# Kernel optimization log

Hardware: AMD Instinct MI355X
Metric: run time of the kernel (lower is better)

## Reference

```python
import jax, jax.numpy as jnp
import numpy as np

N = 50000          # nodes
E = 1_600_000      # edges
H = 64             # agg_hidden (heads=1, concat)
IN = 7             # in_channels
EDIM = 4           # edge_dim
G = 256            # num graphs in batch
FC = 128           # fc_hidden
NC = 2             # num_classes
SLOPE = 0.2        # GATv2 LeakyReLU negative slope


def setup_inputs() -> dict:
    key = jax.random.key(0)
    ks = jax.random.split(key, 24)
    s = 0.1
    d = {
        "x": jax.random.normal(ks[0], (N, IN), dtype=jnp.float32),
        "edge_index": jax.random.randint(ks[1], (2, E), 0, N, dtype=jnp.int32),
        "edge_attr": jax.random.normal(ks[2], (E, EDIM), dtype=jnp.float32),
        "batch": jnp.sort(jax.random.randint(ks[3], (N,), 0, G, dtype=jnp.int32)),
        # GATv2 layer 0 (in=7 -> 64)
        "Wl0": jax.random.normal(ks[4], (IN, H)) * s,
        "bl0": jnp.zeros((H,), jnp.float32),
        "Wr0": jax.random.normal(ks[5], (IN, H)) * s,
        "br0": jnp.zeros((H,), jnp.float32),
        "We0": jax.random.normal(ks[6], (EDIM, H)) * s,
        "att0": jax.random.normal(ks[7], (H,)) * s,
        "bias0": jnp.zeros((H,), jnp.float32),
        # GATv2 layer 1 (64 -> 64)
        "Wl1": jax.random.normal(ks[8], (H, H)) * s,
        "bl1": jnp.zeros((H,), jnp.float32),
        "Wr1": jax.random.normal(ks[9], (H, H)) * s,
        "br1": jnp.zeros((H,), jnp.float32),
        "We1": jax.random.normal(ks[10], (EDIM, H)) * s,
        "att1": jax.random.normal(ks[11], (H,)) * s,
        "bias1": jnp.zeros((H,), jnp.float32),
        # MLP head
        "fc1_w": jax.random.normal(ks[12], (H, FC)) * s,
        "fc1_b": jnp.zeros((FC,), jnp.float32),
        "fc2_w": jax.random.normal(ks[13], (FC, NC)) * s,
        "fc2_b": jnp.zeros((NC,), jnp.float32),
    }
    return d


def _gatv2(x, src, dst, edge_attr, Wl, bl, Wr, br, We, att, bias):
    # GATv2Conv (heads=1, concat=True, edge_dim=EDIM), eval mode (no dropout)
    xl = x @ Wl + bl                         # source-side projection [N,H]
    xr = x @ Wr + br                         # target-side projection [N,H]
    e = xl[src] + xr[dst] + edge_attr @ We   # per-edge pre-activation [E,H]
    score = jax.nn.leaky_relu(e, SLOPE) @ att  # [E]
    # segment softmax over destination nodes
    m = jax.ops.segment_max(score, dst, num_segments=N)
    ex = jnp.exp(score - m[dst])
    den = jax.ops.segment_sum(ex, dst, num_segments=N)
    alpha = ex / (den[dst] + 1e-16)
    out = jax.ops.segment_sum(xl[src] * alpha[:, None], dst, num_segments=N)
    return out + bias


def reference(x, edge_index, edge_attr, batch,
              Wl0, bl0, Wr0, br0, We0, att0, bias0,
              Wl1, bl1, Wr1, br1, We1, att1, bias1,
              fc1_w, fc1_b, fc2_w, fc2_b):
    src, dst = edge_index[0], edge_index[1]
    h = jax.nn.elu(_gatv2(x, src, dst, edge_attr, Wl0, bl0, Wr0, br0, We0, att0, bias0))
    h = jax.nn.elu(_gatv2(h, src, dst, edge_attr, Wl1, bl1, Wr1, br1, We1, att1, bias1))
    # global mean pool over graphs
    sums = jax.ops.segment_sum(h, batch, num_segments=G)
    cnt = jax.ops.segment_sum(jnp.ones((h.shape[0],), h.dtype), batch, num_segments=G)
    g = sums / jnp.maximum(cnt, 1.0)[:, None]      # [G,H]
    g = jax.nn.relu(g @ fc1_w + fc1_b)
    logits = g @ fc2_w + fc2_b
    return jax.nn.log_softmax(logits, axis=1)
```

## Files before the change

### kernel.cpp

```cpp
#include <hip/hip_runtime.h>
#include <hip/hip_fp16.h>

#define N_NODES 50000
#define N_EDGES 1600000
#define H 64
#define IN_CH 7
#define EDIM 4
#define G_GRAPHS 256
#define FC 128
#define NC 2
#define SLOPE 0.2f
#define BSH 6
#define BNODES 64
#define NBUCK ((N_NODES + BNODES - 1) / BNODES)
#define EPB1 8192
#define NB1 ((N_EDGES + EPB1 - 1) / EPB1)
#define PAIR_BLOCKS ((N_NODES * 32 + 255) / 256)

typedef _Float16 h2v __attribute__((ext_vector_type(2)));

__device__ __forceinline__ float fdot2f(h2v a, h2v b, float c) {
#if defined(__has_builtin) && __has_builtin(__builtin_amdgcn_fdot2)
    return __builtin_amdgcn_fdot2(a, b, c, false);
#else
    return c + (float)a[0] * (float)b[0] + (float)a[1] * (float)b[1];
#endif
}

__device__ __forceinline__ float wave_sum_to63(float x) {
    x += __int_as_float(__builtin_amdgcn_update_dpp(0, __float_as_int(x), 0x111, 0xf, 0xf, true));
    x += __int_as_float(__builtin_amdgcn_update_dpp(0, __float_as_int(x), 0x112, 0xf, 0xf, true));
    x += __int_as_float(__builtin_amdgcn_update_dpp(0, __float_as_int(x), 0x114, 0xf, 0xf, true));
    x += __int_as_float(__builtin_amdgcn_update_dpp(0, __float_as_int(x), 0x118, 0xf, 0xf, true));
    x += __int_as_float(__builtin_amdgcn_update_dpp(0, __float_as_int(x), 0x142, 0xf, 0xf, true));
    x += __int_as_float(__builtin_amdgcn_update_dpp(0, __float_as_int(x), 0x143, 0xf, 0xf, true));
    return x;
}
__device__ __forceinline__ float lane63_bcast(float x) {
    return __int_as_float(__builtin_amdgcn_readlane(__float_as_int(x), 63));
}

__global__ __launch_bounds__(256) void front_kernel(
        const int* __restrict__ dst, int* __restrict__ rank1, int* __restrict__ bhist,
        const float* __restrict__ xin,
        const float* __restrict__ Wl0, const float* __restrict__ bl0,
        const float* __restrict__ Wr0, const float* __restrict__ br0,
        __half2* __restrict__ xlh, __half2* __restrict__ xrh,
        const float* __restrict__ We0, const float* __restrict__ We1,
        const float* __restrict__ Wl1, const float* __restrict__ bl1,
        const float* __restrict__ Wr1, const float* __restrict__ br1,
        __half2* __restrict__ weh0, __half2* __restrict__ weh1,
        __half2* __restrict__ wt, float* __restrict__ bb,
        const float* __restrict__ att0, const float* __restrict__ att1,
        __half2* __restrict__ atth0, __half2* __restrict__ atth1) {
    __shared__ int hist[NBUCK];
    int b = blockIdx.x;
    int t = threadIdx.x;
    if (b < NB1) {
        for (int i = t; i < NBUCK; i += 256) hist[i] = 0;
        __syncthreads();
#pragma unroll
        for (int i = 0; i < EPB1 / 256; ++i) {
            int e = b * EPB1 + i * 256 + t;
            if (e < N_EDGES) {
                int k = dst[e] >> BSH;
                rank1[e] = atomicAdd(&hist[k], 1);
            }
        }
        __syncthreads();
        for (int i = t; i < NBUCK; i += 256) bhist[b * NBUCK + i] = hist[i];
    } else if (b < NB1 + PAIR_BLOCKS) {
        int idx = (b - NB1) * 256 + t;
        if (idx < N_NODES * 32) {
            int n = idx >> 5;
            int c = idx & 31;
            const float* xi = xin + n * IN_CH;
            float2 bl2 = ((const float2*)bl0)[c];
            float2 br2 = ((const float2*)br0)[c];
            float al0 = bl2.x, al1 = bl2.y, ar0 = br2.x, ar1 = br2.y;
#pragma unroll
            for (int k = 0; k < IN_CH; ++k) {
                float xv = xi[k];
                float2 wl2 = ((const float2*)(Wl0 + k * H))[c];
                float2 wr2 = ((const float2*)(Wr0 + k * H))[c];
                al0 += xv * wl2.x; al1 += xv * wl2.y;
                ar0 += xv * wr2.x; ar1 += xv * wr2.y;
            }
            xlh[idx] = __floats2half2_rn(al0, al1);
            xrh[idx] = __floats2half2_rn(ar0, ar1);
        }
    } else {
        if (t < 32) {
            for (int k = 0; k < 4; ++k)
                weh0[t * 4 + k] = __floats2half2_rn(We0[k * H + 2 * t], We0[k * H + 2 * t + 1]);
        } else if (t < 64) {
            int c = t - 32;
            for (int k = 0; k < 4; ++k)
                weh1[c * 4 + k] = __floats2half2_rn(We1[k * H + 2 * c], We1[k * H + 2 * c + 1]);
        }
        if (t < 128) {
            const float* W = (t < 64) ? Wl1 : Wr1;
            int c = t & 63;
            for (int kk = 0; kk < 32; ++kk)
                wt[t * 32 + kk] = __floats2half2_rn(W[(2 * kk) * H + c], W[(2 * kk + 1) * H + c]);
            bb[t] = (t < 64) ? bl1[c] : br1[c];
        } else if (t < 160) {
            int c = t - 128;
            atth0[c] = __floats2half2_rn(att0[2 * c], att0[2 * c + 1]);
            atth1[c] = __floats2half2_rn(att1[2 * c], att1[2 * c + 1]);
        }
    }
}

__global__ __launch_bounds__(256) void scan_a_kernel(
        const int* __restrict__ bhist, int* __restrict__ bases, int* __restrict__ btot) {
    __shared__ int lds[256];
    int k = blockIdx.x;
    int t = threadIdx.x;
    int v = (t < NB1) ? bhist[t * NBUCK + k] : 0;
    lds[t] = v;
    __syncthreads();
    for (int off = 1; off < 256; off <<= 1) {
        int x = (t >= off) ? lds[t - off] : 0;
        __syncthreads();
        lds[t] += x;
        __syncthreads();
    }
    if (t < NB1) bases[t * NBUCK + k] = lds[t] - v;
    if (t == NB1 - 1) btot[k] = lds[t];
}

__global__ __launch_bounds__(1024) void scan_b_kernel(
        const int* __restrict__ btot, int* __restrict__ cb_start) {
    __shared__ int lds[1024];
    int t = threadIdx.x;
    int v = (t < NBUCK) ? btot[t] : 0;
    lds[t] = v;
    __syncthreads();
    for (int off = 1; off < 1024; off <<= 1) {
        int x = (t >= off) ? lds[t - off] : 0;
        __syncthreads();
        lds[t] += x;
        __syncthreads();
    }
    if (t < NBUCK) cb_start[t] = lds[t] - v;
    if (t == NBUCK - 1) cb_start[NBUCK] = lds[t];
}

__global__ void coarse_scatter_kernel(const int* __restrict__ src, const int* __restrict__ dst,
                                      const int* __restrict__ rank1, const int* __restrict__ bases,
                                      const int* __restrict__ cb_start,
                                      const float* __restrict__ edge_attr,
                                      int4* __restrict__ tmp) {
    int e = blockIdx.x * blockDim.x + threadIdx.x;
    if (e >= N_EDGES) return;
    int d = dst[e];
    int k = d >> BSH;
    int b = e / EPB1;
    int slot = cb_start[k] + bases[b * NBUCK + k] + rank1[e];
    float4 ea = ((const float4*)edge_attr)[e];
    __half2 h01 = __floats2half2_rn(ea.x, ea.y);
    __half2 h23 = __floats2half2_rn(ea.z, ea.w);
    int4 ent;
    ent.x = src[e];
    ent.y = *reinterpret_cast<int*>(&h01);
    ent.z = *reinterpret_cast<int*>(&h23);
    ent.w = d;
    tmp[slot] = ent;
}

__global__ __launch_bounds__(256) void fine_sort_kernel(
        const int* __restrict__ cb_start, const int4* __restrict__ tmp,
        int4* __restrict__ csr, int* __restrict__ srcs,
        int* __restrict__ row_start) {
    __shared__ int hist2[BNODES];
    __shared__ int cursor[BNODES];
    __shared__ int lds[BNODES];
    int k = blockIdx.x;
    int t = threadIdx.x;
    int beg = cb_start[k], end = cb_start[k + 1];
    if (t < BNODES) hist2[t] = 0;
    __syncthreads();
    for (int i = beg + t; i < end; i += 256)
        atomicAdd(&hist2[tmp[i].w & (BNODES - 1)], 1);
    __syncthreads();
    int v = 0;
    if (t < BNODES) { v = hist2[t]; lds[t] = v; }
    __syncthreads();
    for (int off = 1; off < BNODES; off <<= 1) {
        int x = (t < BNODES && t >= off) ? lds[t - off] : 0;
        __syncthreads();
        if (t < BNODES) lds[t] += x;
        __syncthreads();
    }
    if (t < BNODES) {
        int pre = lds[t] - v;
        cursor[t] = pre;
        int node = (k << BSH) + t;
        if (node <= N_NODES) row_start[node] = beg + pre;
    }
    __syncthreads();
    for (int i = beg + t; i < end; i += 256) {
        int4 ent = tmp[i];
        int slot = beg + atomicAdd(&cursor[ent.w & (BNODES - 1)], 1);
        csr[slot] = ent;
        srcs[slot] = ent.x;
    }
}

__global__ __launch_bounds__(256) void proj1_kernel(
        const float* __restrict__ xin,
        const __half2* __restrict__ wt,
        const float* __restrict__ bb,
        __half2* __restrict__ xlh, __half2* __restrict__ xrh) {
    int g = __builtin_amdgcn_readfirstlane((int)(threadIdx.x >> 6));
    int lane = threadIdx.x & 63;
    int node = blockIdx.x * 64 + lane;
    if (node >= N_NODES) return;

    h2v xrow[32];
    const float4* xp = (const float4*)(xin + node * 64);
#pragma unroll
    for (int q = 0; q < 16; ++q) {
        float4 v = xp[q];
        __half2 a = __floats2half2_rn(v.x, v.y);
        __half2 b = __floats2half2_rn(v.z, v.w);
        xrow[2 * q]     = *reinterpret_cast<h2v*>(&a);
        xrow[2 * q + 1] = *reinterpret_cast<h2v*>(&b);
    }

    __half2* outp = (g < 2) ? xlh : xrh;
    int chbase = g * 32;
    int localbase = (g & 1) * 16;

#pragma unroll
    for (int cp = 0; cp < 16; ++cp) {
        int ch0 = chbase + 2 * cp;
        const h2v* w0 = (const h2v*)(wt + ch0 * 32);
        const h2v* w1 = (const h2v*)(wt + (ch0 + 1) * 32);
        float a0 = bb[ch0], a1 = bb[ch0 + 1];
#pragma unroll
        for (int kk = 0; kk < 32; ++kk) {
            a0 = fdot2f(xrow[kk], w0[kk], a0);
            a1 = fdot2f(xrow[kk], w1[kk], a1);
        }
        outp[node * 32 + localbase + cp] = __floats2half2_rn(a0, a1);
    }
}

__global__ __launch_bounds__(256) void score_kernel(
        const int4* __restrict__ csr,
        const __half2* __restrict__ xlh, const __half2* __restrict__ xrh,
        const __half2* __restrict__ weh, const __half2* __restrict__ atth,
        float* __restrict__ score) {
    __shared__ __half2 sweh[128];
    __shared__ __half2 satth[32];
    int t = threadIdx.x;
    if (t < 128) sweh[t] = weh[t];
    else if (t < 160) satth[t - 128] = atth[t - 128];
    __syncthreads();

    int e = blockIdx.x * 64 + (t >> 2);
    int sub = t & 3;
    int4 ent = csr[e];
    __half2 ea01 = *reinterpret_cast<__half2*>(&ent.y);
    __half2 ea23 = *reinterpret_cast<__half2*>(&ent.z);
    __half2 e0 = __half2half2(__low2half(ea01));
    __half2 e1 = __half2half2(__high2half(ea01));
    __half2 e2 = __half2half2(__low2half(ea23));
    __half2 e3 = __half2half2(__high2half(ea23));
    const h2v sl = { (_Float16)SLOPE, (_Float16)SLOPE };

    const int4* xa = (const int4*)(xlh + (size_t)ent.x * 32) + sub * 2;
    const int4* xb = (const int4*)(xrh + (size_t)ent.w * 32) + sub * 2;
    int4 va[2], vb[2];
    va[0] = xa[0]; va[1] = xa[1];
    vb[0] = xb[0]; vb[1] = xb[1];
    const __half2* ha = reinterpret_cast<const __half2*>(va);
    const __half2* hc = reinterpret_cast<const __half2*>(vb);

    float acc = 0.f;
#pragma unroll
    for (int j = 0; j < 8; ++j) {
        int c = sub * 8 + j;
        __half2 v2 = __hadd2(ha[j], hc[j]);
        v2 = __hfma2(e0, sweh[c * 4 + 0], v2);
        v2 = __hfma2(e1, sweh[c * 4 + 1], v2);
        v2 = __hfma2(e2, sweh[c * 4 + 2], v2);
        v2 = __hfma2(e3, sweh[c * 4 + 3], v2);
        h2v vv = *reinterpret_cast<h2v*>(&v2);
        h2v Lv = __builtin_elementwise_max(vv, sl * vv);
        __half2 av = satth[c];
        acc = fdot2f(Lv, *reinterpret_cast<h2v*>(&av), acc);
    }
    acc += __shfl_xor(acc, 1, 64);
    acc += __shfl_xor(acc, 2, 64);
    if (sub == 0) score[e] = acc;
}

__global__ __launch_bounds__(256) void agg_kernel(
        const int* __restrict__ row_start,
        const int* __restrict__ srcs,
        const float* __restrict__ score,
        const __half2* __restrict__ xlh,
        const float* __restrict__ bias,
        float* __restrict__ out) {
    int wave = (blockIdx.x * blockDim.x + threadIdx.x) >> 6;
    if (wave >= N_NODES) return;
    int lane = threadIdx.x & 63;
    int q = lane & 15;
    int grp = lane >> 4;
    int d = wave;
    int beg = __builtin_amdgcn_readfirstlane(row_start[d]);
    int end = __builtin_amdgcn_readfirstlane(row_start[d + 1]);

    const int2* xl2 = (const int2*)xlh;

    float l_lane = 0.f;
    float a0 = 0.f, a1 = 0.f, a2 = 0.f, a3 = 0.f;

    for (int cbeg = beg; cbeg < end; cbeg += 64) {
        int n = end - cbeg;
        int nn = min(n, 64);
        float sc = score[cbeg + lane];
        float p = __expf(sc);
        p = (lane < n) ? p : 0.f;
        l_lane += p;
        int sv = srcs[cbeg + lane];

        for (int j = 0; j < nn; j += 4) {
            int e = j + grp;
            bool ok = e < nn;
            int esel = ok ? e : 0;
            int s = __shfl(sv, esel, 64);
            float pe = __shfl(p, esel, 64);
            pe = ok ? pe : 0.f;
            int2 xw = xl2[(size_t)s * 16 + q];
            __half2 h0 = *reinterpret_cast<__half2*>(&xw.x);
            __half2 h1 = *reinterpret_cast<__half2*>(&xw.y);
            float2 f0 = __half22float2(h0);
            float2 f1 = __half22float2(h1);
            a0 += pe * f0.x; a1 += pe * f0.y;
            a2 += pe * f1.x; a3 += pe * f1.y;
        }
    }

    a0 += __shfl_xor(a0, 16, 64); a0 += __shfl_xor(a0, 32, 64);
    a1 += __shfl_xor(a1, 16, 64); a1 += __shfl_xor(a1, 32, 64);
    a2 += __shfl_xor(a2, 16, 64); a2 += __shfl_xor(a2, 32, 64);
    a3 += __shfl_xor(a3, 16, 64); a3 += __shfl_xor(a3, 32, 64);
    float l = lane63_bcast(wave_sum_to63(l_lane));
    if (grp == 0) {
        float inv = 1.f / (l + 1e-16f);
        float4 b4 = ((const float4*)bias)[q];
        float o0 = a0 * inv + b4.x;
        float o1 = a1 * inv + b4.y;
        float o2 = a2 * inv + b4.z;
        float o3 = a3 * inv + b4.w;
        o0 = o0 > 0.f ? o0 : expm1f(o0);
        o1 = o1 > 0.f ? o1 : expm1f(o1);
        o2 = o2 > 0.f ? o2 : expm1f(o2);
        o3 = o3 > 0.f ? o3 : expm1f(o3);
        ((float4*)out)[d * 16 + q] = float4{o0, o1, o2, o3};
    }
}

__global__ __launch_bounds__(256) void pool_head_kernel(
        const float* __restrict__ h, const int* __restrict__ batch,
        const float* __restrict__ fc1w, const float* __restrict__ fc1b,
        const float* __restrict__ fc2w, const float* __restrict__ fc2b,
        float* __restrict__ out) {
    int g = blockIdx.x;
    int lo = 0, hi = N_NODES;
    while (lo < hi) { int mid = (lo + hi) >> 1; if (batch[mid] < g) lo = mid + 1; else hi = mid; }
    int start = lo;
    hi = N_NODES;
    while (lo < hi) { int mid = (lo + hi) >> 1; if (batch[mid] < g + 1) lo = mid + 1; else hi = mid; }
    int end = lo;

    int lane = threadIdx.x & 63;
    int w = threadIdx.x >> 6;
    float s = 0.f;
    for (int n = start + w; n < end; n += 4) s += h[n * H + lane];
    __shared__ float red[4][H];
    __shared__ float gv[H];
    __shared__ float f[FC];
    __shared__ float lg[NC];
    red[w][lane] = s;
    __syncthreads();
    if (w == 0) {
        float tot = red[0][lane] + red[1][lane] + red[2][lane] + red[3][lane];
        gv[lane] = tot / fmaxf((float)(end - start), 1.f);
    }
    __syncthreads();
    int t = threadIdx.x;
    if (t < FC) {
        float acc = fc1b[t];
#pragma unroll 16
        for (int k = 0; k < H; ++k) acc += gv[k] * fc1w[k * FC + t];
        f[t] = fmaxf(acc, 0.f);
    }
    __syncthreads();
    if (t < NC) {
        float a = fc2b[t];
        for (int k = 0; k < FC; ++k) a += f[k] * fc2w[k * NC + t];
        lg[t] = a;
    }
    __syncthreads();
    if (t < NC) {
        float mx = fmaxf(lg[0], lg[1]);
        float lse = mx + logf(expf(lg[0] - mx) + expf(lg[1] - mx));
        out[g * NC + t] = lg[t] - lse;
    }
}

extern "C" void kernel_launch(void* const* d_in, const int* in_sizes, int n_in,
                              void* d_out, int out_size, void* d_ws, size_t ws_size,
                              hipStream_t stream) {
    const float* x         = (const float*)d_in[0];
    const int*   edge_idx  = (const int*)d_in[1];
    const float* edge_attr = (const float*)d_in[2];
    const int*   batch     = (const int*)d_in[3];
    const float* Wl0  = (const float*)d_in[4];
    const float* bl0  = (const float*)d_in[5];
    const float* Wr0  = (const float*)d_in[6];
    const float* br0  = (const float*)d_in[7];
    const float* We0  = (const float*)d_in[8];
    const float* att0 = (const float*)d_in[9];
    const float* bias0= (const float*)d_in[10];
    const float* Wl1  = (const float*)d_in[11];
    const float* bl1  = (const float*)d_in[12];
    const float* Wr1  = (const float*)d_in[13];
    const float* br1  = (const float*)d_in[14];
    const float* We1  = (const float*)d_in[15];
    const float* att1 = (const float*)d_in[16];
    const float* bias1= (const float*)d_in[17];
    const float* fc1w = (const float*)d_in[18];
    const float* fc1b = (const float*)d_in[19];
    const float* fc2w = (const float*)d_in[20];
    const float* fc2b = (const float*)d_in[21];

    __half2* xlh    = (__half2*)d_ws;
    __half2* xrh    = xlh + N_NODES * 32;
    float* C        = (float*)(xrh + N_NODES * 32);
    float* escore   = C + N_NODES * 64;
    float* pad      = escore + N_EDGES;
    int4*  tmp      = (int4*)C;
    int4*  csr      = (int4*)(pad + N_EDGES);
    int*   srcs     = (int*)(csr + N_EDGES);
    int*   row_start= srcs + N_EDGES;
    int*   rank1    = row_start + N_NODES + 1;
    int*   bhist    = rank1 + N_EDGES;
    int*   bases    = bhist + NB1 * NBUCK;
    int*   btot     = bases + NB1 * NBUCK;
    int*   cb_start = btot + NBUCK;
    __half2* weh0   = (__half2*)(cb_start + NBUCK + 1);
    __half2* weh1   = weh0 + 128;
    __half2* wt1    = weh1 + 128;
    float* bb1      = (float*)(wt1 + 128 * 32);
    __half2* atth0  = (__half2*)(bb1 + 128);
    __half2* atth1  = atth0 + 32;

    const int* src = edge_idx;
    const int* dst = edge_idx + N_EDGES;

    const int edgeBlocks  = (N_EDGES + 255) / 256;
    const int scoreBlocks = N_EDGES / 64;
    const int waveBlocks  = (N_NODES * 64 + 255) / 256;
    const int p1Blocks    = (N_NODES + 63) / 64;
    const int frontBlocks = NB1 + PAIR_BLOCKS + 1;

    front_kernel<<<frontBlocks, 256, 0, stream>>>(dst, rank1, bhist,
                                                  x, Wl0, bl0, Wr0, br0, xlh, xrh,
                                                  We0, We1, Wl1, bl1, Wr1, br1,
                                                  weh0, weh1, wt1, bb1,
                                                  att0, att1, atth0, atth1);
    scan_a_kernel<<<NBUCK, 256, 0, stream>>>(bhist, bases, btot);
    scan_b_kernel<<<1, 1024, 0, stream>>>(btot, cb_start);
    coarse_scatter_kernel<<<edgeBlocks, 256, 0, stream>>>(src, dst, rank1, bases, cb_start,
                                                          edge_attr, tmp);
    fine_sort_kernel<<<NBUCK, 256, 0, stream>>>(cb_start, tmp, csr, srcs, row_start);

    score_kernel<<<scoreBlocks, 256, 0, stream>>>(csr, xlh, xrh, weh0, atth0, escore);
    agg_kernel<<<waveBlocks, 256, 0, stream>>>(row_start, srcs, escore, xlh, bias0, C);

    proj1_kernel<<<p1Blocks, 256, 0, stream>>>(C, wt1, bb1, xlh, xrh);
    score_kernel<<<scoreBlocks, 256, 0, stream>>>(csr, xlh, xrh, weh1, atth1, escore);
    agg_kernel<<<waveBlocks, 256, 0, stream>>>(row_start, srcs, escore, xlh, bias1, C);

    pool_head_kernel<<<G_GRAPHS, 256, 0, stream>>>(C, batch, fc1w, fc1b, fc2w, fc2b, (float*)d_out);
}
```

Measured before the change: 379.8 us.

## Replace rank-based bucket scatter with global atomic cursors and byte keys

The per-block bucket histogram, rank array and two-level scan are replaced by global bucket counts accumulated atomically, a single scan, and per-bucket atomic cursors in the scatter kernel. The scatter also writes a compact byte key per slot so the fine sort's histogram pass reads one byte instead of a 16-byte entry. This removes the rank array traffic and one kernel launch. In exchange it adds global atomic contention and makes edge order within a node nondeterministic, which can change float summation order.

```diff
diff --git a/kernel.cpp b/kernel.cpp
--- a/kernel.cpp
+++ b/kernel.cpp
@@ -41,7 +41,7 @@
 }
 
 __global__ __launch_bounds__(256) void front_kernel(
-        const int* __restrict__ dst, int* __restrict__ rank1, int* __restrict__ bhist,
+        const int* __restrict__ dst, int* __restrict__ bcnt,
         const float* __restrict__ xin,
         const float* __restrict__ Wl0, const float* __restrict__ bl0,
         const float* __restrict__ Wr0, const float* __restrict__ br0,
@@ -62,13 +62,14 @@
 #pragma unroll
         for (int i = 0; i < EPB1 / 256; ++i) {
             int e = b * EPB1 + i * 256 + t;
-            if (e < N_EDGES) {
-                int k = dst[e] >> BSH;
-                rank1[e] = atomicAdd(&hist[k], 1);
-            }
-        }
-        __syncthreads();
-        for (int i = t; i < NBUCK; i += 256) bhist[b * NBUCK + i] = hist[i];
+            if (e < N_EDGES)
+                atomicAdd(&hist[dst[e] >> BSH], 1);
+        }
+        __syncthreads();
+        for (int i = t; i < NBUCK; i += 256) {
+            int v = hist[i];
+            if (v) atomicAdd(&bcnt[i], v);
+        }
     } else if (b < NB1 + PAIR_BLOCKS) {
         int idx = (b - NB1) * 256 + t;
         if (idx < N_NODES * 32) {
@@ -112,29 +113,11 @@
     }
 }
 
-__global__ __launch_bounds__(256) void scan_a_kernel(
-        const int* __restrict__ bhist, int* __restrict__ bases, int* __restrict__ btot) {
-    __shared__ int lds[256];
-    int k = blockIdx.x;
-    int t = threadIdx.x;
-    int v = (t < NB1) ? bhist[t * NBUCK + k] : 0;
-    lds[t] = v;
-    __syncthreads();
-    for (int off = 1; off < 256; off <<= 1) {
-        int x = (t >= off) ? lds[t - off] : 0;
-        __syncthreads();
-        lds[t] += x;
-        __syncthreads();
-    }
-    if (t < NB1) bases[t * NBUCK + k] = lds[t] - v;
-    if (t == NB1 - 1) btot[k] = lds[t];
-}
-
-__global__ __launch_bounds__(1024) void scan_b_kernel(
-        const int* __restrict__ btot, int* __restrict__ cb_start) {
+__global__ __launch_bounds__(1024) void bucket_scan_kernel(
+        const int* __restrict__ bcnt, int* __restrict__ cb_start, int* __restrict__ cursor) {
     __shared__ int lds[1024];
     int t = threadIdx.x;
-    int v = (t < NBUCK) ? btot[t] : 0;
+    int v = (t < NBUCK) ? bcnt[t] : 0;
     lds[t] = v;
     __syncthreads();
     for (int off = 1; off < 1024; off <<= 1) {
@@ -143,21 +126,24 @@
         lds[t] += x;
         __syncthreads();
     }
-    if (t < NBUCK) cb_start[t] = lds[t] - v;
+    if (t < NBUCK) {
+        int ex = lds[t] - v;
+        cb_start[t] = ex;
+        cursor[t] = ex;
+    }
     if (t == NBUCK - 1) cb_start[NBUCK] = lds[t];
 }
 
 __global__ void coarse_scatter_kernel(const int* __restrict__ src, const int* __restrict__ dst,
-                                      const int* __restrict__ rank1, const int* __restrict__ bases,
-                                      const int* __restrict__ cb_start,
+                                      int* __restrict__ cursor,
                                       const float* __restrict__ edge_attr,
-                                      int4* __restrict__ tmp) {
+                                      int4* __restrict__ tmp,
+                                      unsigned char* __restrict__ dstb) {
     int e = blockIdx.x * blockDim.x + threadIdx.x;
     if (e >= N_EDGES) return;
     int d = dst[e];
     int k = d >> BSH;
-    int b = e / EPB1;
-    int slot = cb_start[k] + bases[b * NBUCK + k] + rank1[e];
+    int slot = atomicAdd(&cursor[k], 1);
     float4 ea = ((const float4*)edge_attr)[e];
     __half2 h01 = __floats2half2_rn(ea.x, ea.y);
     __half2 h23 = __floats2half2_rn(ea.z, ea.w);
@@ -167,10 +153,12 @@
     ent.z = *reinterpret_cast<int*>(&h23);
     ent.w = d;
     tmp[slot] = ent;
+    dstb[slot] = (unsigned char)(d & (BNODES - 1));
 }
 
 __global__ __launch_bounds__(256) void fine_sort_kernel(
         const int* __restrict__ cb_start, const int4* __restrict__ tmp,
+        const unsigned char* __restrict__ dstb,
         int4* __restrict__ csr, int* __restrict__ srcs,
         int* __restrict__ row_start) {
     __shared__ int hist2[BNODES];
@@ -182,7 +170,7 @@
     if (t < BNODES) hist2[t] = 0;
     __syncthreads();
     for (int i = beg + t; i < end; i += 256)
-        atomicAdd(&hist2[tmp[i].w & (BNODES - 1)], 1);
+        atomicAdd(&hist2[dstb[i]], 1);
     __syncthreads();
     int v = 0;
     if (t < BNODES) { v = hist2[t]; lds[t] = v; }
@@ -449,12 +437,11 @@
     int4*  csr      = (int4*)(pad + N_EDGES);
     int*   srcs     = (int*)(csr + N_EDGES);
     int*   row_start= srcs + N_EDGES;
-    int*   rank1    = row_start + N_NODES + 1;
-    int*   bhist    = rank1 + N_EDGES;
-    int*   bases    = bhist + NB1 * NBUCK;
-    int*   btot     = bases + NB1 * NBUCK;
-    int*   cb_start = btot + NBUCK;
-    __half2* weh0   = (__half2*)(cb_start + NBUCK + 1);
+    unsigned char* dstb = (unsigned char*)(row_start + N_NODES + 1);
+    int*   bcnt     = (int*)(dstb + N_EDGES);
+    int*   cb_start = bcnt + NBUCK;
+    int*   cursor   = cb_start + NBUCK + 1;
+    __half2* weh0   = (__half2*)(cursor + NBUCK);
     __half2* weh1   = weh0 + 128;
     __half2* wt1    = weh1 + 128;
     float* bb1      = (float*)(wt1 + 128 * 32);
@@ -470,16 +457,16 @@
     const int p1Blocks    = (N_NODES + 63) / 64;
     const int frontBlocks = NB1 + PAIR_BLOCKS + 1;
 
-    front_kernel<<<frontBlocks, 256, 0, stream>>>(dst, rank1, bhist,
+    hipMemsetAsync(bcnt, 0, NBUCK * sizeof(int), stream);
+    front_kernel<<<frontBlocks, 256, 0, stream>>>(dst, bcnt,
                                                   x, Wl0, bl0, Wr0, br0, xlh, xrh,
                                                   We0, We1, Wl1, bl1, Wr1, br1,
                                                   weh0, weh1, wt1, bb1,
                                                   att0, att1, atth0, atth1);
-    scan_a_kernel<<<NBUCK, 256, 0, stream>>>(bhist, bases, btot);
-    scan_b_kernel<<<1, 1024, 0, stream>>>(btot, cb_start);
-    coarse_scatter_kernel<<<edgeBlocks, 256, 0, stream>>>(src, dst, rank1, bases, cb_start,
-                                                          edge_attr, tmp);
-    fine_sort_kernel<<<NBUCK, 256, 0, stream>>>(cb_start, tmp, csr, srcs, row_start);
+    bucket_scan_kernel<<<1, 1024, 0, stream>>>(bcnt, cb_start, cursor);
+    coarse_scatter_kernel<<<edgeBlocks, 256, 0, stream>>>(src, dst, cursor,
+                                                          edge_attr, tmp, dstb);
+    fine_sort_kernel<<<NBUCK, 256, 0, stream>>>(cb_start, tmp, dstb, csr, srcs, row_start);
 
     score_kernel<<<scoreBlocks, 256, 0, stream>>>(csr, xlh, xrh, weh0, atth0, escore);
     agg_kernel<<<waveBlocks, 256, 0, stream>>>(row_start, srcs, escore, xlh, bias0, C);
```

After: 729.0 us. +92.0%, slower.
